# Optimization experiments

Hardware: AMD Instinct MI355X
Metric: run time of the kernel (lower is better)

## Reference

```python
import jax, jax.numpy as jnp
import numpy as np

B, T, F, H = 2048, 256, 64, 128


def setup_inputs() -> dict:
    key = jax.random.key(0)
    ks = jax.random.split(key, 9)
    s = 0.1  # small init scale for stable recurrence
    return {
        "x": jax.random.normal(ks[0], (B, T, F), dtype=jnp.float32),
        "W_ih": jax.random.normal(ks[1], (4 * H, F), dtype=jnp.float32) * s,
        "W_hh": jax.random.normal(ks[2], (4 * H, H), dtype=jnp.float32) * s,
        "b_ih": jax.random.normal(ks[3], (4 * H,), dtype=jnp.float32) * s,
        "b_hh": jax.random.normal(ks[4], (4 * H,), dtype=jnp.float32) * s,
        "W1": jax.random.normal(ks[5], (32, H), dtype=jnp.float32) * s,
        "b1": jax.random.normal(ks[6], (32,), dtype=jnp.float32) * s,
        "W2": jax.random.normal(ks[7], (1, 32), dtype=jnp.float32) * s,
        "b2": jax.random.normal(ks[8], (1,), dtype=jnp.float32) * s,
    }


def reference(x, W_ih, W_hh, b_ih, b_hh, W1, b1, W2, b2):
    # Single-layer LSTM (PyTorch gate order i, f, g, o), take last hidden state.
    Bsz, Tlen, _ = x.shape
    Hdim = W_hh.shape[1]
    xt = jnp.swapaxes(x, 0, 1)  # [T, B, F]
    bias = b_ih + b_hh  # [4H]

    def step(carry, xb):
        h, c = carry
        gates = xb @ W_ih.T + h @ W_hh.T + bias  # [B, 4H]
        i, f, g, o = jnp.split(gates, 4, axis=-1)
        i = jax.nn.sigmoid(i)
        f = jax.nn.sigmoid(f)
        g = jnp.tanh(g)
        o = jax.nn.sigmoid(o)
        c = f * c + i * g
        h = o * jnp.tanh(c)
        return (h, c), None

    h0 = jnp.zeros((Bsz, Hdim), dtype=x.dtype)
    c0 = jnp.zeros((Bsz, Hdim), dtype=x.dtype)
    (h_last, _), _ = jax.lax.scan(step, (h0, c0), xt)

    # head: Linear(H,32) -> ReLU -> Linear(32,1) -> Sigmoid -> squeeze(-1)
    z = jax.nn.relu(h_last @ W1.T + b1)
    return jax.nn.sigmoid(z @ W2.T + b2)[:, 0]
```

## Files before the change

### kernel.cpp

```cpp
#include <hip/hip_runtime.h>


#define Bsz   2048
#define Tlen  256
#define Fdim  64
#define Hdim  128
#define ROWS  8
#define NTH   512
#define TILE_E 512
#define NKT   6
#define BUF_E (NKT * TILE_E)

using bf16x8 = __attribute__((ext_vector_type(8))) __bf16;
using f32x4  = __attribute__((ext_vector_type(4))) float;

__device__ __forceinline__ float fast_rcp(float x) {
#if __has_builtin(__builtin_amdgcn_rcpf)
    return __builtin_amdgcn_rcpf(x);
#else
    return 1.0f / x;
#endif
}
__device__ __forceinline__ float fast_exp2(float x) {
#if __has_builtin(__builtin_amdgcn_exp2f)
    return __builtin_amdgcn_exp2f(x);
#else
    return exp2f(x);
#endif
}
__device__ __forceinline__ float fsig(float x) {
    return fast_rcp(1.0f + fast_exp2(-1.4426950408889634f * x));
}
__device__ __forceinline__ float ftanh(float x) {
    float e = fast_exp2(-2.8853900817779268f * x);
    return (1.0f - e) * fast_rcp(1.0f + e);
}

__device__ __forceinline__ int frag_elem(int row, int k) {
    return (k >> 5) * TILE_E + ((((k >> 3) & 3) * 16 + row) * 8) + (k & 7);
}

__global__ __launch_bounds__(NTH, 2)
void lstm_fused(const float* __restrict__ x,
                const float* __restrict__ W_ih,
                const float* __restrict__ W_hh,
                const float* __restrict__ b_ih,
                const float* __restrict__ b_hh,
                const float* __restrict__ W1,
                const float* __restrict__ b1,
                const float* __restrict__ W2,
                const float* __restrict__ b2,
                float* __restrict__ out)
{
    __shared__ __bf16 Abuf[2][BUF_E];
    __shared__ float  hlast[ROWS * Hdim];
    __shared__ float  zbuf[ROWS * 32];

    const int tid  = threadIdx.x;
    const int w    = tid >> 6;
    const int lane = tid & 63;
    const int quad = lane >> 4;
    const int l16  = lane & 15;
    const int b0   = blockIdx.x * ROWS;

    bf16x8 bw[NKT][4];
    #pragma unroll
    for (int kt = 0; kt < NKT; ++kt) {
        const int k0 = kt * 32 + quad * 8;
        #pragma unroll
        for (int g = 0; g < 4; ++g) {
            const int n = g * Hdim + w * 16 + l16;
            const float* p = (kt < 2) ? (W_ih + (size_t)n * Fdim + k0)
                                      : (W_hh + (size_t)n * Hdim + (k0 - Fdim));
            float4 lo = *(const float4*)p;
            float4 hi = *(const float4*)(p + 4);
            bf16x8 r;
            r[0]=(__bf16)lo.x; r[1]=(__bf16)lo.y; r[2]=(__bf16)lo.z; r[3]=(__bf16)lo.w;
            r[4]=(__bf16)hi.x; r[5]=(__bf16)hi.y; r[6]=(__bf16)hi.z; r[7]=(__bf16)hi.w;
            bw[kt][g] = r;
        }
    }
    float biasv[4];
    #pragma unroll
    for (int g = 0; g < 4; ++g) {
        const int n = g * Hdim + w * 16 + l16;
        biasv[g] = b_ih[n] + b_hh[n];
    }

    const bool sx_on  = tid < 256;
    const int  sx_row = tid & 7;
    const int  sx_fp  = (tid >> 3) & 31;
    const int  f0     = 2 * sx_fp;
    const float* xrp  = x + (size_t)(b0 + sx_row) * (Tlen * Fdim) + f0;
    const int sx_e0 = frag_elem(sx_row,     f0);
    const int sx_e1 = frag_elem(sx_row + 8, f0);

    const int r0  = (quad >> 1) * 2;
    const int brb = (quad & 1) * 4 + r0;
    const int hc  = 16 * w + l16;
    const int h_e0a = frag_elem(brb,     Fdim + hc);
    const int h_e0b = frag_elem(brb + 8, Fdim + hc);
    const int h_e1a = frag_elem(brb + 1,     Fdim + hc);
    const int h_e1b = frag_elem(brb + 1 + 8, Fdim + hc);

    #pragma unroll
    for (int i = 0; i < BUF_E / NTH; ++i)
        Abuf[0][tid + i * NTH] = (__bf16)0.0f;
    float2 xpre = make_float2(0.f, 0.f);
    __syncthreads();
    if (sx_on) {
        float2 v0 = *(const float2*)xrp;
        __bf16 a0[2] = {(__bf16)v0.x, (__bf16)v0.y};
        *(uint*)&Abuf[0][sx_e0] = *(uint*)a0;
        *(uint*)&Abuf[0][sx_e1] = *(uint*)a0;
        xpre = *(const float2*)(xrp + Fdim);
    }
    __syncthreads();

    float cc0 = 0.0f, cc1 = 0.0f;

    for (int t = 0; t < Tlen; ++t) {
        const int p = t & 1;
        const __bf16* rb = Abuf[p];
        __bf16*      wbf = (__bf16*)Abuf[1 - p];

        bf16x8 af[NKT];
        #pragma unroll
        for (int kt = 0; kt < NKT; ++kt)
            af[kt] = *(const bf16x8*)&rb[kt * TILE_E + lane * 8];

        float2 xnext = make_float2(0.f, 0.f);
        if (sx_on && (t + 2) < Tlen)
            xnext = *(const float2*)(xrp + (size_t)(t + 2) * Fdim);

        f32x4 acc[4];
        #pragma unroll
        for (int g = 0; g < 4; ++g)
            acc[g] = (f32x4){biasv[g], biasv[g], biasv[g], biasv[g]};
        #pragma unroll
        for (int kt = 0; kt < NKT; ++kt) {
            #pragma unroll
            for (int g = 0; g < 4; ++g)
                acc[g] = __builtin_amdgcn_mfma_f32_16x16x32_bf16(af[kt], bw[kt][g], acc[g], 0, 0, 0);
        }

        {
            float iv = fsig(acc[0][r0]);
            float fv = fsig(acc[1][r0]);
            float gv = ftanh(acc[2][r0]);
            float ov = fsig(acc[3][r0]);
            cc0 = fv * cc0 + iv * gv;
            float h = ov * ftanh(cc0);
            __bf16 hb = (__bf16)h;
            wbf[h_e0a] = hb;
            wbf[h_e0b] = hb;
            if (t == Tlen - 1) hlast[brb * Hdim + hc] = h;
        }
        {
            float iv = fsig(acc[0][r0 + 1]);
            float fv = fsig(acc[1][r0 + 1]);
            float gv = ftanh(acc[2][r0 + 1]);
            float ov = fsig(acc[3][r0 + 1]);
            cc1 = fv * cc1 + iv * gv;
            float h = ov * ftanh(cc1);
            __bf16 hb = (__bf16)h;
            wbf[h_e1a] = hb;
            wbf[h_e1b] = hb;
            if (t == Tlen - 1) hlast[(brb + 1) * Hdim + hc] = h;
        }

        if (sx_on && (t + 1) < Tlen) {
            __bf16 xa[2] = {(__bf16)xpre.x, (__bf16)xpre.y};
            *(uint*)&wbf[sx_e0] = *(uint*)xa;
            *(uint*)&wbf[sx_e1] = *(uint*)xa;
        }
        xpre = xnext;
        __syncthreads();
    }

    if (tid < ROWS * 32) {
        const int b = tid >> 5, n = tid & 31;
        const float4* w4 = (const float4*)(W1 + n * Hdim);
        const float4* h4 = (const float4*)(hlast + b * Hdim);
        float s = b1[n];
        #pragma unroll
        for (int kk = 0; kk < Hdim / 4; ++kk) {
            float4 wv = w4[kk];
            float4 hv = h4[kk];
            s += wv.x * hv.x + wv.y * hv.y + wv.z * hv.z + wv.w * hv.w;
        }
        zbuf[b * 32 + n] = fmaxf(s, 0.0f);
    }
    __syncthreads();
    if (tid < ROWS) {
        float s = b2[0];
        #pragma unroll
        for (int n = 0; n < 32; ++n) s += zbuf[tid * 32 + n] * W2[n];
        out[b0 + tid] = fsig(s);
    }
}

extern "C" void kernel_launch(void* const* d_in, const int* in_sizes, int n_in,
                              void* d_out, int out_size, void* d_ws, size_t ws_size,
                              hipStream_t stream) {
    const float* x    = (const float*)d_in[0];
    const float* W_ih = (const float*)d_in[1];
    const float* W_hh = (const float*)d_in[2];
    const float* b_ih = (const float*)d_in[3];
    const float* b_hh = (const float*)d_in[4];
    const float* W1   = (const float*)d_in[5];
    const float* b1   = (const float*)d_in[6];
    const float* W2   = (const float*)d_in[7];
    const float* b2   = (const float*)d_in[8];
    float* out = (float*)d_out;

    dim3 grid(Bsz / ROWS), block(NTH);
    lstm_fused<<<grid, block, 0, stream>>>(x, W_ih, W_hh, b_ih, b_hh, W1, b1, W2, b2, out);
}
```

Before: 376.0 us.

## Load x fragments directly into registers and shrink LDS buffer to hidden state only

Each lane now loads its MFMA A-fragment of x straight from global memory into registers one step ahead, instead of staging x through shared memory. The LDS double buffer holds only the hidden state. The duplicated writes of h into mirrored rows 8-15 are removed, and reads use a row index masked to 0-7. The gate MFMAs are split into two halves so the i/f activations can overlap the g/o matrix work. This cuts LDS traffic and footprint per step, at the cost of more global loads per lane, since each x element is fetched by many waves, plus extra registers.

```diff
diff --git a/kernel.cpp b/kernel.cpp
--- a/kernel.cpp
+++ b/kernel.cpp
@@ -8,8 +8,7 @@
 #define ROWS  8
 #define NTH   512
 #define TILE_E 512
-#define NKT   6
-#define BUF_E (NKT * TILE_E)
+#define HBUF_E (4 * TILE_E)
 
 using bf16x8 = __attribute__((ext_vector_type(8))) __bf16;
 using f32x4  = __attribute__((ext_vector_type(4))) float;
@@ -36,8 +35,15 @@
     return (1.0f - e) * fast_rcp(1.0f + e);
 }
 
-__device__ __forceinline__ int frag_elem(int row, int k) {
-    return (k >> 5) * TILE_E + ((((k >> 3) & 3) * 16 + row) * 8) + (k & 7);
+__device__ __forceinline__ bf16x8 cvt8(float4 a, float4 b) {
+    bf16x8 r;
+    r[0]=(__bf16)a.x; r[1]=(__bf16)a.y; r[2]=(__bf16)a.z; r[3]=(__bf16)a.w;
+    r[4]=(__bf16)b.x; r[5]=(__bf16)b.y; r[6]=(__bf16)b.z; r[7]=(__bf16)b.w;
+    return r;
+}
+
+__device__ __forceinline__ int helem(int row, int hk) {
+    return (hk >> 5) * TILE_E + ((((hk >> 3) & 3) * 16 + row) * 8) + (hk & 7);
 }
 
 __global__ __launch_bounds__(NTH, 2)
@@ -52,7 +58,7 @@
                 const float* __restrict__ b2,
                 float* __restrict__ out)
 {
-    __shared__ __bf16 Abuf[2][BUF_E];
+    __shared__ __bf16 Hbuf[2][HBUF_E];
     __shared__ float  hlast[ROWS * Hdim];
     __shared__ float  zbuf[ROWS * 32];
 
@@ -63,9 +69,9 @@
     const int l16  = lane & 15;
     const int b0   = blockIdx.x * ROWS;
 
-    bf16x8 bw[NKT][4];
+    bf16x8 bwx[2][4], bwh[4][4];
     #pragma unroll
-    for (int kt = 0; kt < NKT; ++kt) {
+    for (int kt = 0; kt < 6; ++kt) {
         const int k0 = kt * 32 + quad * 8;
         #pragma unroll
         for (int g = 0; g < 4; ++g) {
@@ -74,10 +80,8 @@
                                       : (W_hh + (size_t)n * Hdim + (k0 - Fdim));
             float4 lo = *(const float4*)p;
             float4 hi = *(const float4*)(p + 4);
-            bf16x8 r;
-            r[0]=(__bf16)lo.x; r[1]=(__bf16)lo.y; r[2]=(__bf16)lo.z; r[3]=(__bf16)lo.w;
-            r[4]=(__bf16)hi.x; r[5]=(__bf16)hi.y; r[6]=(__bf16)hi.z; r[7]=(__bf16)hi.w;
-            bw[kt][g] = r;
+            bf16x8 r = cvt8(lo, hi);
+            if (kt < 2) bwx[kt][g] = r; else bwh[kt - 2][g] = r;
         }
     }
     float biasv[4];
@@ -87,33 +91,27 @@
         biasv[g] = b_ih[n] + b_hh[n];
     }
 
-    const bool sx_on  = tid < 256;
-    const int  sx_row = tid & 7;
-    const int  sx_fp  = (tid >> 3) & 31;
-    const int  f0     = 2 * sx_fp;
-    const float* xrp  = x + (size_t)(b0 + sx_row) * (Tlen * Fdim) + f0;
-    const int sx_e0 = frag_elem(sx_row,     f0);
-    const int sx_e1 = frag_elem(sx_row + 8, f0);
+    const float* xlp = x + (size_t)(b0 + (l16 & 7)) * (Tlen * Fdim) + quad * 8;
+
+    const int hread = (quad * 16 + (l16 & 7)) * 8;
 
     const int r0  = (quad >> 1) * 2;
     const int brb = (quad & 1) * 4 + r0;
     const int hc  = 16 * w + l16;
-    const int h_e0a = frag_elem(brb,     Fdim + hc);
-    const int h_e0b = frag_elem(brb + 8, Fdim + hc);
-    const int h_e1a = frag_elem(brb + 1,     Fdim + hc);
-    const int h_e1b = frag_elem(brb + 1 + 8, Fdim + hc);
+    const int hw0 = helem(brb,     hc);
+    const int hw1 = helem(brb + 1, hc);
 
     #pragma unroll
-    for (int i = 0; i < BUF_E / NTH; ++i)
-        Abuf[0][tid + i * NTH] = (__bf16)0.0f;
-    float2 xpre = make_float2(0.f, 0.f);
-    __syncthreads();
-    if (sx_on) {
-        float2 v0 = *(const float2*)xrp;
-        __bf16 a0[2] = {(__bf16)v0.x, (__bf16)v0.y};
-        *(uint*)&Abuf[0][sx_e0] = *(uint*)a0;
-        *(uint*)&Abuf[0][sx_e1] = *(uint*)a0;
-        xpre = *(const float2*)(xrp + Fdim);
+    for (int i = 0; i < (2 * HBUF_E) / NTH; ++i)
+        ((__bf16*)Hbuf)[tid + i * NTH] = (__bf16)0.0f;
+    bf16x8 xf0, xf1;
+    {
+        float4 a0 = *(const float4*)(xlp);
+        float4 a1 = *(const float4*)(xlp + 4);
+        float4 a2 = *(const float4*)(xlp + 32);
+        float4 a3 = *(const float4*)(xlp + 36);
+        xf0 = cvt8(a0, a1);
+        xf1 = cvt8(a2, a3);
     }
     __syncthreads();
 
@@ -121,60 +119,64 @@
 
     for (int t = 0; t < Tlen; ++t) {
         const int p = t & 1;
-        const __bf16* rb = Abuf[p];
-        __bf16*      wbf = (__bf16*)Abuf[1 - p];
-
-        bf16x8 af[NKT];
-        #pragma unroll
-        for (int kt = 0; kt < NKT; ++kt)
-            af[kt] = *(const bf16x8*)&rb[kt * TILE_E + lane * 8];
-
-        float2 xnext = make_float2(0.f, 0.f);
-        if (sx_on && (t + 2) < Tlen)
-            xnext = *(const float2*)(xrp + (size_t)(t + 2) * Fdim);
+        const __bf16* rb = Hbuf[p];
+        __bf16*      wb  = (__bf16*)Hbuf[1 - p];
+
+        bf16x8 hf[4];
+        #pragma unroll
+        for (int kt = 0; kt < 4; ++kt)
+            hf[kt] = *(const bf16x8*)&rb[kt * TILE_E + hread];
+
+        float4 xn0, xn1, xn2, xn3;
+        const bool ldx = (t + 1) < Tlen;
+        if (ldx) {
+            const float* xp = xlp + (size_t)(t + 1) * Fdim;
+            xn0 = *(const float4*)(xp);
+            xn1 = *(const float4*)(xp + 4);
+            xn2 = *(const float4*)(xp + 32);
+            xn3 = *(const float4*)(xp + 36);
+        }
 
         f32x4 acc[4];
         #pragma unroll
-        for (int g = 0; g < 4; ++g)
+        for (int g = 0; g < 2; ++g) {
             acc[g] = (f32x4){biasv[g], biasv[g], biasv[g], biasv[g]};
-        #pragma unroll
-        for (int kt = 0; kt < NKT; ++kt) {
+            acc[g] = __builtin_amdgcn_mfma_f32_16x16x32_bf16(xf0, bwx[0][g], acc[g], 0, 0, 0);
+            acc[g] = __builtin_amdgcn_mfma_f32_16x16x32_bf16(xf1, bwx[1][g], acc[g], 0, 0, 0);
             #pragma unroll
-            for (int g = 0; g < 4; ++g)
-                acc[g] = __builtin_amdgcn_mfma_f32_16x16x32_bf16(af[kt], bw[kt][g], acc[g], 0, 0, 0);
-        }
-
-        {
-            float iv = fsig(acc[0][r0]);
-            float fv = fsig(acc[1][r0]);
-            float gv = ftanh(acc[2][r0]);
-            float ov = fsig(acc[3][r0]);
-            cc0 = fv * cc0 + iv * gv;
-            float h = ov * ftanh(cc0);
-            __bf16 hb = (__bf16)h;
-            wbf[h_e0a] = hb;
-            wbf[h_e0b] = hb;
-            if (t == Tlen - 1) hlast[brb * Hdim + hc] = h;
-        }
-        {
-            float iv = fsig(acc[0][r0 + 1]);
-            float fv = fsig(acc[1][r0 + 1]);
-            float gv = ftanh(acc[2][r0 + 1]);
-            float ov = fsig(acc[3][r0 + 1]);
-            cc1 = fv * cc1 + iv * gv;
-            float h = ov * ftanh(cc1);
-            __bf16 hb = (__bf16)h;
-            wbf[h_e1a] = hb;
-            wbf[h_e1b] = hb;
-            if (t == Tlen - 1) hlast[(brb + 1) * Hdim + hc] = h;
-        }
-
-        if (sx_on && (t + 1) < Tlen) {
-            __bf16 xa[2] = {(__bf16)xpre.x, (__bf16)xpre.y};
-            *(uint*)&wbf[sx_e0] = *(uint*)xa;
-            *(uint*)&wbf[sx_e1] = *(uint*)xa;
-        }
-        xpre = xnext;
+            for (int kt = 0; kt < 4; ++kt)
+                acc[g] = __builtin_amdgcn_mfma_f32_16x16x32_bf16(hf[kt], bwh[kt][g], acc[g], 0, 0, 0);
+        }
+        float iv0 = fsig(acc[0][r0]), iv1 = fsig(acc[0][r0 + 1]);
+        float fv0 = fsig(acc[1][r0]), fv1 = fsig(acc[1][r0 + 1]);
+        #pragma unroll
+        for (int g = 2; g < 4; ++g) {
+            acc[g] = (f32x4){biasv[g], biasv[g], biasv[g], biasv[g]};
+            acc[g] = __builtin_amdgcn_mfma_f32_16x16x32_bf16(xf0, bwx[0][g], acc[g], 0, 0, 0);
+            acc[g] = __builtin_amdgcn_mfma_f32_16x16x32_bf16(xf1, bwx[1][g], acc[g], 0, 0, 0);
+            #pragma unroll
+            for (int kt = 0; kt < 4; ++kt)
+                acc[g] = __builtin_amdgcn_mfma_f32_16x16x32_bf16(hf[kt], bwh[kt][g], acc[g], 0, 0, 0);
+        }
+        float gv0 = ftanh(acc[2][r0]), gv1 = ftanh(acc[2][r0 + 1]);
+        float ov0 = fsig(acc[3][r0]),  ov1 = fsig(acc[3][r0 + 1]);
+
+        cc0 = fv0 * cc0 + iv0 * gv0;
+        float h0 = ov0 * ftanh(cc0);
+        cc1 = fv1 * cc1 + iv1 * gv1;
+        float h1 = ov1 * ftanh(cc1);
+
+        wb[hw0] = (__bf16)h0;
+        wb[hw1] = (__bf16)h1;
+        if (t == Tlen - 1) {
+            hlast[brb * Hdim + hc]       = h0;
+            hlast[(brb + 1) * Hdim + hc] = h1;
+        }
+
+        if (ldx) {
+            xf0 = cvt8(xn0, xn1);
+            xf1 = cvt8(xn2, xn3);
+        }
         __syncthreads();
     }
 
```

New measurement: 583.0 us. 55.0% more time.

## Split input projection off the recurrent critical path and precompute it a step ahead

Applied to the files above, without the earlier changes.

Splits the gate matmul into an input part (x @ W_ih) and a recurrent part (h @ W_hh). The input projection for step t+1 is computed with MFMA after the activations of step t, off the h-dependency chain. This shortens the serial chain at each step from six K-tiles to four. The x staging pipeline is shifted one step further ahead, and extra registers are needed to hold the precomputed accumulators.

```diff
diff --git a/kernel.cpp b/kernel.cpp
--- a/kernel.cpp
+++ b/kernel.cpp
@@ -34,6 +34,13 @@
 __device__ __forceinline__ float ftanh(float x) {
     float e = fast_exp2(-2.8853900817779268f * x);
     return (1.0f - e) * fast_rcp(1.0f + e);
+}
+
+__device__ __forceinline__ bf16x8 cvt8(float4 a, float4 b) {
+    bf16x8 r;
+    r[0]=(__bf16)a.x; r[1]=(__bf16)a.y; r[2]=(__bf16)a.z; r[3]=(__bf16)a.w;
+    r[4]=(__bf16)b.x; r[5]=(__bf16)b.y; r[6]=(__bf16)b.z; r[7]=(__bf16)b.w;
+    return r;
 }
 
 __device__ __forceinline__ int frag_elem(int row, int k) {
@@ -63,7 +70,7 @@
     const int l16  = lane & 15;
     const int b0   = blockIdx.x * ROWS;
 
-    bf16x8 bw[NKT][4];
+    bf16x8 bwx[2][4], bwh[4][4];
     #pragma unroll
     for (int kt = 0; kt < NKT; ++kt) {
         const int k0 = kt * 32 + quad * 8;
@@ -74,10 +81,8 @@
                                       : (W_hh + (size_t)n * Hdim + (k0 - Fdim));
             float4 lo = *(const float4*)p;
             float4 hi = *(const float4*)(p + 4);
-            bf16x8 r;
-            r[0]=(__bf16)lo.x; r[1]=(__bf16)lo.y; r[2]=(__bf16)lo.z; r[3]=(__bf16)lo.w;
-            r[4]=(__bf16)hi.x; r[5]=(__bf16)hi.y; r[6]=(__bf16)hi.z; r[7]=(__bf16)hi.w;
-            bw[kt][g] = r;
+            bf16x8 r = cvt8(lo, hi);
+            if (kt < 2) bwx[kt][g] = r; else bwh[kt - 2][g] = r;
         }
     }
     float biasv[4];
@@ -98,22 +103,37 @@
     const int r0  = (quad >> 1) * 2;
     const int brb = (quad & 1) * 4 + r0;
     const int hc  = 16 * w + l16;
-    const int h_e0a = frag_elem(brb,     Fdim + hc);
-    const int h_e0b = frag_elem(brb + 8, Fdim + hc);
+    const int h_e0a = frag_elem(brb,         Fdim + hc);
+    const int h_e0b = frag_elem(brb + 8,     Fdim + hc);
     const int h_e1a = frag_elem(brb + 1,     Fdim + hc);
     const int h_e1b = frag_elem(brb + 1 + 8, Fdim + hc);
 
     #pragma unroll
     for (int i = 0; i < BUF_E / NTH; ++i)
         Abuf[0][tid + i * NTH] = (__bf16)0.0f;
+    __syncthreads();
     float2 xpre = make_float2(0.f, 0.f);
-    __syncthreads();
     if (sx_on) {
-        float2 v0 = *(const float2*)xrp;
-        __bf16 a0[2] = {(__bf16)v0.x, (__bf16)v0.y};
-        *(uint*)&Abuf[0][sx_e0] = *(uint*)a0;
-        *(uint*)&Abuf[0][sx_e1] = *(uint*)a0;
-        xpre = *(const float2*)(xrp + Fdim);
+        float2 v1 = *(const float2*)(xrp + Fdim);
+        __bf16 a1[2] = {(__bf16)v1.x, (__bf16)v1.y};
+        *(uint*)&Abuf[0][sx_e0] = *(uint*)a1;
+        *(uint*)&Abuf[0][sx_e1] = *(uint*)a1;
+        xpre = *(const float2*)(xrp + 2 * Fdim);
+    }
+    f32x4 xacc[4];
+    {
+        const float* x0p = x + (size_t)(b0 + (l16 & 7)) * (Tlen * Fdim) + quad * 8;
+        float4 a0 = *(const float4*)(x0p);
+        float4 a1 = *(const float4*)(x0p + 4);
+        float4 a2 = *(const float4*)(x0p + 32);
+        float4 a3 = *(const float4*)(x0p + 36);
+        bf16x8 xi0 = cvt8(a0, a1), xi1 = cvt8(a2, a3);
+        #pragma unroll
+        for (int g = 0; g < 4; ++g) {
+            xacc[g] = (f32x4){biasv[g], biasv[g], biasv[g], biasv[g]};
+            xacc[g] = __builtin_amdgcn_mfma_f32_16x16x32_bf16(xi0, bwx[0][g], xacc[g], 0, 0, 0);
+            xacc[g] = __builtin_amdgcn_mfma_f32_16x16x32_bf16(xi1, bwx[1][g], xacc[g], 0, 0, 0);
+        }
     }
     __syncthreads();
 
@@ -124,24 +144,25 @@
         const __bf16* rb = Abuf[p];
         __bf16*      wbf = (__bf16*)Abuf[1 - p];
 
-        bf16x8 af[NKT];
-        #pragma unroll
-        for (int kt = 0; kt < NKT; ++kt)
-            af[kt] = *(const bf16x8*)&rb[kt * TILE_E + lane * 8];
+        bf16x8 hf[4];
+        #pragma unroll
+        for (int kt = 0; kt < 4; ++kt)
+            hf[kt] = *(const bf16x8*)&rb[(2 + kt) * TILE_E + lane * 8];
+        bf16x8 xf0 = *(const bf16x8*)&rb[lane * 8];
+        bf16x8 xf1 = *(const bf16x8*)&rb[TILE_E + lane * 8];
 
         float2 xnext = make_float2(0.f, 0.f);
-        if (sx_on && (t + 2) < Tlen)
-            xnext = *(const float2*)(xrp + (size_t)(t + 2) * Fdim);
+        if (sx_on && (t + 3) < Tlen)
+            xnext = *(const float2*)(xrp + (size_t)(t + 3) * Fdim);
 
         f32x4 acc[4];
         #pragma unroll
-        for (int g = 0; g < 4; ++g)
-            acc[g] = (f32x4){biasv[g], biasv[g], biasv[g], biasv[g]};
-        #pragma unroll
-        for (int kt = 0; kt < NKT; ++kt) {
+        for (int g = 0; g < 4; ++g) acc[g] = xacc[g];
+        #pragma unroll
+        for (int kt = 0; kt < 4; ++kt) {
             #pragma unroll
             for (int g = 0; g < 4; ++g)
-                acc[g] = __builtin_amdgcn_mfma_f32_16x16x32_bf16(af[kt], bw[kt][g], acc[g], 0, 0, 0);
+                acc[g] = __builtin_amdgcn_mfma_f32_16x16x32_bf16(hf[kt], bwh[kt][g], acc[g], 0, 0, 0);
         }
 
         {
@@ -169,7 +190,16 @@
             if (t == Tlen - 1) hlast[(brb + 1) * Hdim + hc] = h;
         }
 
-        if (sx_on && (t + 1) < Tlen) {
+        if ((t + 1) < Tlen) {
+            #pragma unroll
+            for (int g = 0; g < 4; ++g) {
+                xacc[g] = (f32x4){biasv[g], biasv[g], biasv[g], biasv[g]};
+                xacc[g] = __builtin_amdgcn_mfma_f32_16x16x32_bf16(xf0, bwx[0][g], xacc[g], 0, 0, 0);
+                xacc[g] = __builtin_amdgcn_mfma_f32_16x16x32_bf16(xf1, bwx[1][g], xacc[g], 0, 0, 0);
+            }
+        }
+
+        if (sx_on && (t + 2) < Tlen) {
             __bf16 xa[2] = {(__bf16)xpre.x, (__bf16)xpre.y};
             *(uint*)&wbf[sx_e0] = *(uint*)xa;
             *(uint*)&wbf[sx_e1] = *(uint*)xa;
```

Measured after the change: 365.1 us. -2.9%, faster.
